# Performance work log

Measured on AMD Instinct MI355X. Metric: run time of the kernel, lower is better.

The kernel has to match this reference:

```python
import jax, jax.numpy as jnp
import numpy as np

GDEP = 3
ALPHA = 0.05
C_IN = 32
C_OUT = 32


def setup_inputs() -> dict:
    key = jax.random.key(0)
    k1, k2, k3, k4 = jax.random.split(key, 4)
    B, C, V, L = 16, C_IN, 512, 168
    x = jax.random.normal(k1, (B, C, V, L), dtype=jnp.float32)
    adj = jax.random.uniform(k2, (V, V), dtype=jnp.float32)
    fan_in = (GDEP + 1) * C_IN  # Conv2d 1x1: kaiming-uniform-ish init
    bound = 1.0 / np.sqrt(fan_in)
    W = jax.random.uniform(k3, (C_OUT, fan_in), minval=-bound, maxval=bound, dtype=jnp.float32)
    b = jax.random.uniform(k4, (C_OUT,), minval=-bound, maxval=bound, dtype=jnp.float32)
    return {"x": x, "adj": adj, "W": W, "b": b}


def reference(x, adj, W, b):
    V = adj.shape[0]
    a = adj + jnp.eye(V, dtype=adj.dtype)
    d = a.sum(axis=1)
    a = a / d[:, None]                      # row-normalized adjacency [V, V]
    h = x
    outs = [h]
    for _ in range(GDEP):                   # small fixed depth loop
        prop = jnp.einsum('ncvl,vw->ncwl', h, a)
        h = ALPHA * x + (1.0 - ALPHA) * prop
        outs.append(h)
    ho = jnp.concatenate(outs, axis=1)      # [B, (gdep+1)*C, V, L]
    # 1x1 conv == channel contraction
    out = jnp.einsum('bcvl,oc->bovl', ho, W) + b[None, :, None, None]
    return out
```

## Files before the change

kernel.cpp:

```cpp
#include <hip/hip_runtime.h>

#define V 512
#define L 168
#define PLANE 86016
#define CHSTRIDE 2752512
#define B_ 16
#define HDR4 (1u << 22)

typedef __attribute__((ext_vector_type(8))) short s16x8;
typedef __attribute__((ext_vector_type(4))) float f32x4;
typedef unsigned short u16;

__device__ inline short f2bf(float f) {
    unsigned u = __builtin_bit_cast(unsigned, f);
    u += 0x7FFF + ((u >> 16) & 1);
    return (short)(u >> 16);
}
__device__ inline float bf2f(u16 s) {
    return __builtin_bit_cast(float, ((unsigned)s) << 16);
}
__device__ inline void gll16(const u16* g, u16* lds) {
    __builtin_amdgcn_global_load_lds(
        (const __attribute__((address_space(1))) void*)g,
        (__attribute__((address_space(3))) void*)lds, 16, 0, 0);
}

__global__ __launch_bounds__(256) void prep2(const float* __restrict__ adj,
                                             const float* __restrict__ W,
                                             u16* __restrict__ M1,
                                             u16* __restrict__ ANb,
                                             u16* __restrict__ Wb) {
    if (blockIdx.x == V) {
        const float al = 0.05f, be = 0.95f;
        for (int i = threadIdx.x; i < 1024; i += 256) {
            const int o = i >> 5, c = i & 31;
            const float w0 = W[o * 128 + c];
            const float w1 = W[o * 128 + 32 + c];
            const float w2 = W[o * 128 + 64 + c];
            const float w3 = W[o * 128 + 96 + c];
            Wb[o * 128 + c]      = f2bf(w0 + al * (w1 + w2 + w3));
            Wb[o * 128 + 32 + c] = f2bf(be * (w1 + al * (w2 + w3)));
            Wb[o * 128 + 64 + c] = f2bf(be * be * (w2 + al * w3));
            Wb[o * 128 + 96 + c] = f2bf(be * be * be * w3);
        }
        return;
    }
    const int v = blockIdx.x;
    float s = 0.f;
    for (int w = threadIdx.x; w < V; w += 256)
        s += adj[v * V + w] + (w == v ? 1.f : 0.f);
    __shared__ float red[256];
    red[threadIdx.x] = s;
    __syncthreads();
    for (int off = 128; off > 0; off >>= 1) {
        if ((int)threadIdx.x < off) red[threadIdx.x] += red[threadIdx.x + off];
        __syncthreads();
    }
    const float inv = 1.f / red[0];
    for (int w = threadIdx.x; w < V; w += 256) {
        const short q = f2bf((adj[v * V + w] + (w == v ? 1.f : 0.f)) * inv);
        M1[w * V + v] = q;
        ANb[v * V + w] = q;
    }
}

__global__ __launch_bounds__(256) void powk(const u16* __restrict__ X,
                                            const u16* __restrict__ ANb,
                                            u16* __restrict__ OUT) {
    const int w0 = (blockIdx.x >> 3) * 64, v0 = (blockIdx.x & 7) * 64;
    const int tid = threadIdx.x, lane = tid & 63, wave = tid >> 6;
    const int colb = lane & 15, kg = lane >> 4;
    f32x4 acc[4];
#pragma unroll
    for (int i = 0; i < 4; i++) acc[i] = (f32x4){0.f, 0.f, 0.f, 0.f};
#pragma unroll 4
    for (int kk = 0; kk < 16; kk++) {
        const int u = kk * 32 + kg * 8;
        const s16x8 bfr = *(const s16x8*)&ANb[(size_t)(v0 + wave * 16 + colb) * 512 + u];
#pragma unroll
        for (int mt = 0; mt < 4; mt++) {
            const s16x8 afr = *(const s16x8*)&X[(size_t)(w0 + mt * 16 + colb) * 512 + u];
            acc[mt] = __builtin_amdgcn_mfma_f32_16x16x32_bf16(afr, bfr, acc[mt], 0, 0, 0);
        }
    }
#pragma unroll
    for (int mt = 0; mt < 4; mt++)
#pragma unroll
        for (int r = 0; r < 4; r++)
            OUT[(size_t)(w0 + mt * 16 + kg * 4 + r) * 512 + v0 + wave * 16 + colb] =
                (u16)f2bf(acc[mt][r]);
}

__global__ __launch_bounds__(256) void cvtT(const float* __restrict__ x,
                                            u16* __restrict__ xa) {
    const int b = blockIdx.z >> 5, c = blockIdx.z & 31;
    const int v0 = blockIdx.y * 64, l0 = blockIdx.x * 64;
    const int tid = threadIdx.x;
    __shared__ float T[64][65];
    const float* xp = x + (size_t)b * CHSTRIDE + (size_t)c * PLANE;
    u16* xo = xa + (size_t)b * CHSTRIDE;
#pragma unroll
    for (int rep = 0; rep < 16; rep++) {
        const int idx = rep * 256 + tid;
        const int vv = idx >> 6, ll = idx & 63;
        if (l0 + ll < L) T[vv][ll] = xp[(size_t)(v0 + vv) * L + l0 + ll];
    }
    __syncthreads();
#pragma unroll
    for (int rep = 0; rep < 16; rep++) {
        const int idx = rep * 256 + tid;
        const int ll = idx >> 6, vv = idx & 63;
        if (l0 + ll < L)
            xo[(size_t)((l0 + ll) * 32 + c) * 512 + v0 + vv] = f2bf(T[vv][ll]);
    }
}

__global__ __launch_bounds__(256, 2) void propOut(const u16* __restrict__ xa,
                                                  const u16* __restrict__ AS,
                                                  const u16* __restrict__ Wb,
                                                  const float* __restrict__ bias,
                                                  u16* __restrict__ tmpb) {
    const int b = blockIdx.z;
    const int logical = (blockIdx.x & 7) * 21 + (blockIdx.x >> 3);
    const int ntile = logical >> 2, wq = logical & 3;
    const int n0 = ntile * 128, w0 = wq * 128, l0 = ntile * 4;
    const int tid = threadIdx.x, lane = tid & 63, wave = tid >> 6;
    const int wm = wave >> 1, wn = wave & 1;
    const int colb = lane & 15, kg = lane >> 4;
    __shared__ __align__(16) u16 SH[2][16384];
    u16* flat = &SH[0][0];
    const size_t sB = (size_t)b * CHSTRIDE;
    const u16* srcb = xa + sB;

    f32x4 aco[2][8];
#pragma unroll
    for (int i = 0; i < 2; i++)
#pragma unroll
        for (int j = 0; j < 8; j++) aco[i][j] = (f32x4){0.f, 0.f, 0.f, 0.f};

#pragma unroll
    for (int pf = 0; pf < 8; pf++) {
        s16x8 bfr;
#pragma unroll
        for (int j = 0; j < 8; j++)
            bfr[j] = (short)srcb[(size_t)(n0 + wave * 32 + kg * 8 + j) * 512 +
                                 w0 + pf * 16 + colb];
#pragma unroll
        for (int mt = 0; mt < 2; mt++) {
            const s16x8 afr = *(const s16x8*)&Wb[(mt * 16 + colb) * 128 + kg * 8];
            aco[mt][pf] = __builtin_amdgcn_mfma_f32_16x16x32_bf16(afr, bfr, aco[mt][pf], 0, 0, 0);
        }
    }

#define STAGE(T, BUF, AK)                                                         \
    {                                                                             \
        const int v0s = (T) * 64;                                                 \
        _Pragma("unroll") for (int i = 0; i < 4; i++) {                           \
            const int cc = wave * 4 + i, oct = cc >> 1, half = cc & 1;            \
            const int row = half * 64 + lane;                                     \
            gll16(&AK[(size_t)(w0 + row) * 512 + v0s + oct * 8],                  \
                  &SH[BUF][oct * 1024 + half * 512]);                             \
            gll16(&srcb[(size_t)(n0 + row) * 512 + v0s + oct * 8],                \
                  &SH[BUF][8192 + oct * 1024 + half * 512]);                      \
        }                                                                         \
    }

#define MFMASTEP(BUF)                                                             \
    _Pragma("unroll") for (int kk = 0; kk < 2; kk++) {                            \
        const int cq = kk * 4 + kg;                                               \
        s16x8 afr[4], bfr[4];                                                     \
        _Pragma("unroll") for (int mt = 0; mt < 4; mt++)                          \
            afr[mt] = *(const s16x8*)&SH[BUF][cq * 1024 +                         \
                                             (wm * 64 + mt * 16 + colb) * 8];     \
        _Pragma("unroll") for (int nt = 0; nt < 4; nt++)                          \
            bfr[nt] = *(const s16x8*)&SH[BUF][8192 + cq * 1024 +                  \
                                             (wn * 64 + nt * 16 + colb) * 8];     \
        _Pragma("unroll") for (int mt = 0; mt < 4; mt++)                          \
            _Pragma("unroll") for (int nt = 0; nt < 4; nt++)                      \
                acc[mt][nt] = __builtin_amdgcn_mfma_f32_16x16x32_bf16(            \
                    afr[mt], bfr[nt], acc[mt][nt], 0, 0, 0);                      \
    }

#define PASS(KP)                                                                  \
    {                                                                             \
        const u16* Ak = AS + (size_t)((KP) - 1) * 262144;                         \
        f32x4 acc[4][4];                                                          \
        _Pragma("unroll") for (int i = 0; i < 4; i++)                             \
            _Pragma("unroll") for (int j = 0; j < 4; j++)                         \
                acc[i][j] = (f32x4){0.f, 0.f, 0.f, 0.f};                          \
        STAGE(0, 0, Ak);                                                          \
        __syncthreads();                                                          \
        _Pragma("unroll") for (int t = 0; t < 8; t++) {                           \
            const int buf = t & 1;                                                \
            if (t < 7) STAGE(t + 1, buf ^ 1, Ak);                                 \
            __builtin_amdgcn_s_setprio(1);                                        \
            MFMASTEP(buf);                                                        \
            __builtin_amdgcn_s_setprio(0);                                        \
            __syncthreads();                                                      \
        }                                                                         \
                              \
        _Pragma("unroll") for (int mt = 0; mt < 4; mt++) {                        \
            const int wr = wm * 64 + mt * 16 + kg * 4;                            \
            _Pragma("unroll") for (int nt = 0; nt < 4; nt++) {                    \
                const int nn = wn * 64 + nt * 16 + colb;                          \
                _Pragma("unroll") for (int r = 0; r < 4; r++)                     \
                    flat[(wr + r) * 136 + nn] = (u16)f2bf(acc[mt][nt][r]);        \
            }                                                                     \
        }                                                                         \
        __syncthreads();                                                          \
                               \
        _Pragma("unroll") for (int pf = 0; pf < 8; pf++) {                        \
            const s16x8 bfr = *(const s16x8*)&flat[(pf * 16 + colb) * 136 +       \
                                                   wave * 32 + kg * 8];           \
            _Pragma("unroll") for (int mt = 0; mt < 2; mt++) {                    \
                const s16x8 afr = *(const s16x8*)&Wb[(mt * 16 + colb) * 128 +     \
                                                     (KP) * 32 + kg * 8];         \
                aco[mt][pf] = __builtin_amdgcn_mfma_f32_16x16x32_bf16(            \
                    afr, bfr, aco[mt][pf], 0, 0, 0);                              \
            }                                                                     \
        }                                                                         \
        __syncthreads();                                                          \
    }

    PASS(1)
    PASS(2)
    PASS(3)
#undef PASS
#undef MFMASTEP
#undef STAGE

#pragma unroll
    for (int mt = 0; mt < 2; mt++)
#pragma unroll
        for (int pf = 0; pf < 8; pf++)
#pragma unroll
            for (int r = 0; r < 4; r++) {
                const int o = mt * 16 + kg * 4 + r;
                tmpb[sB + (size_t)o * PLANE + (size_t)(l0 + wave) * 512 +
                     w0 + pf * 16 + colb] = (u16)f2bf(bias[o] + aco[mt][pf][r]);
            }
}

__global__ __launch_bounds__(256) void transT_b(const u16* __restrict__ tmpb,
                                                float* __restrict__ out) {
    const int o = blockIdx.y, b = blockIdx.z;
    const int vt = blockIdx.x / 3, lt = blockIdx.x % 3;
    const int v0 = vt * 64, l0 = lt * 64;
    const int tid = threadIdx.x;
    __shared__ float T[64][65];
    const u16* tp = tmpb + (size_t)b * CHSTRIDE + (size_t)o * PLANE;
    float* op = out + (size_t)b * CHSTRIDE + (size_t)o * PLANE;
#pragma unroll
    for (int rep = 0; rep < 16; rep++) {
        const int idx = rep * 256 + tid;
        const int ll = idx >> 6, vv = idx & 63;
        if (l0 + ll < L) T[ll][vv] = bf2f(tp[(size_t)(l0 + ll) * 512 + v0 + vv]);
    }
    __syncthreads();
#pragma unroll
    for (int rep = 0; rep < 16; rep++) {
        const int idx = rep * 256 + tid;
        const int vv = idx >> 6, ll = idx & 63;
        if (l0 + ll < L) op[(size_t)(v0 + vv) * L + l0 + ll] = T[ll][vv];
    }
}

extern "C" void kernel_launch(void* const* d_in, const int* in_sizes, int n_in,
                              void* d_out, int out_size, void* d_ws, size_t ws_size,
                              hipStream_t stream) {
    const float* x = (const float*)d_in[0];
    const float* adj = (const float*)d_in[1];
    const float* W = (const float*)d_in[2];
    const float* bias = (const float*)d_in[3];
    float* out = (float*)d_out;

    u16* AS = (u16*)d_ws;
    u16* M1 = AS;
    u16* M2 = AS + 262144;
    u16* M3 = AS + 2 * 262144;
    u16* ANb = AS + 3 * 262144;
    u16* Wb = AS + 4 * 262144;
    u16* hbuf = (u16*)((char*)d_ws + HDR4);

    prep2<<<V + 1, 256, 0, stream>>>(adj, W, M1, ANb, Wb);
    powk<<<64, 256, 0, stream>>>(M1, ANb, M2);
    powk<<<64, 256, 0, stream>>>(M2, ANb, M3);

    const size_t avail = ws_size > HDR4 ? ws_size - HDR4 : 0;
    int nbc = (int)(avail / ((size_t)4 * CHSTRIDE));
    if (nbc < 1) nbc = 1;
    if (nbc > B_) nbc = B_;

    for (int b0 = 0; b0 < B_; b0 += nbc) {
        const int nb = (B_ - b0 < nbc) ? (B_ - b0) : nbc;
        const float* xb = x + (size_t)b0 * CHSTRIDE;
        float* outb = out + (size_t)b0 * CHSTRIDE;
        u16* xa = hbuf;
        u16* tmpb = hbuf + (size_t)nbc * CHSTRIDE;

        cvtT<<<dim3(3, 8, nb * 32), 256, 0, stream>>>(xb, xa);
        propOut<<<dim3(168, 1, nb), 256, 0, stream>>>(xa, AS, Wb, bias, tmpb);
        transT_b<<<dim3(24, 32, nb), 256, 0, stream>>>(tmpb, outb);
    }
}
```

Baseline: 462.2 us.

## Fuse three adjacency-power passes into one K loop sharing the x tile

Replaces the three sequential propagation GEMM passes (one per adjacency power) with a single K loop. Each step loads the x tile once and multiplies it against all three power matrices, accumulating into three register accumulator sets. This cuts global and LDS traffic on the shared operand by a factor of three. In exchange it drops double-buffering, so loads are no longer overlapped with MFMA work, and holding 48 accumulator vectors greatly raises register pressure, which may cause spills or lower occupancy under the 2-blocks-per-CU launch bound.

Measured after the change: 515.8 us. +11.6%, slower.

```diff
diff --git a/kernel.cpp b/kernel.cpp
--- a/kernel.cpp
+++ b/kernel.cpp
@@ -115,11 +115,11 @@
     }
 }
 
-__global__ __launch_bounds__(256, 2) void propOut(const u16* __restrict__ xa,
-                                                  const u16* __restrict__ AS,
-                                                  const u16* __restrict__ Wb,
-                                                  const float* __restrict__ bias,
-                                                  u16* __restrict__ tmpb) {
+__global__ __launch_bounds__(256, 2) void propOut2(const u16* __restrict__ xa,
+                                                   const u16* __restrict__ AS,
+                                                   const u16* __restrict__ Wb,
+                                                   const float* __restrict__ bias,
+                                                   u16* __restrict__ tmpb) {
     const int b = blockIdx.z;
     const int logical = (blockIdx.x & 7) * 21 + (blockIdx.x >> 3);
     const int ntile = logical >> 2, wq = logical & 3;
@@ -127,10 +127,87 @@
     const int tid = threadIdx.x, lane = tid & 63, wave = tid >> 6;
     const int wm = wave >> 1, wn = wave & 1;
     const int colb = lane & 15, kg = lane >> 4;
-    __shared__ __align__(16) u16 SH[2][16384];
-    u16* flat = &SH[0][0];
+    __shared__ __align__(16) u16 SHf[32768];
     const size_t sB = (size_t)b * CHSTRIDE;
     const u16* srcb = xa + sB;
+
+    f32x4 acc1[4][4], acc2[4][4], acc3[4][4];
+#pragma unroll
+    for (int i = 0; i < 4; i++)
+#pragma unroll
+        for (int j = 0; j < 4; j++) {
+            acc1[i][j] = (f32x4){0.f, 0.f, 0.f, 0.f};
+            acc2[i][j] = acc1[i][j];
+            acc3[i][j] = acc1[i][j];
+        }
+
+    const u16* gsrc = (wave == 3) ? srcb + (size_t)n0 * 512
+                                  : AS + (size_t)wave * 262144 + (size_t)w0 * 512;
+    u16* ldst = &SHf[wave * 8192];
+
+    for (int t = 0; t < 8; ++t) {
+        __syncthreads();
+#pragma unroll
+        for (int oh = 0; oh < 16; ++oh) {
+            const int oct = oh >> 1, h = oh & 1;
+            gll16(gsrc + (size_t)(h * 64 + lane) * 512 + t * 64 + oct * 8,
+                  ldst + oct * 1024 + h * 512 + lane * 8);
+        }
+        __syncthreads();
+        __builtin_amdgcn_s_setprio(1);
+#pragma unroll
+        for (int kk = 0; kk < 2; ++kk) {
+            const int cq = kk * 4 + kg;
+            s16x8 bfr[4];
+#pragma unroll
+            for (int nt = 0; nt < 4; nt++)
+                bfr[nt] = *(const s16x8*)&SHf[24576 + cq * 1024 +
+                                              (wn * 64 + nt * 16 + colb) * 8];
+#pragma unroll
+            for (int mt = 0; mt < 4; mt++) {
+                const int aoff = cq * 1024 + (wm * 64 + mt * 16 + colb) * 8;
+                const s16x8 a1 = *(const s16x8*)&SHf[aoff];
+                const s16x8 a2 = *(const s16x8*)&SHf[8192 + aoff];
+                const s16x8 a3 = *(const s16x8*)&SHf[16384 + aoff];
+#pragma unroll
+                for (int nt = 0; nt < 4; nt++) {
+                    acc1[mt][nt] = __builtin_amdgcn_mfma_f32_16x16x32_bf16(a1, bfr[nt],
+                                                                           acc1[mt][nt], 0, 0, 0);
+                    acc2[mt][nt] = __builtin_amdgcn_mfma_f32_16x16x32_bf16(a2, bfr[nt],
+                                                                           acc2[mt][nt], 0, 0, 0);
+                    acc3[mt][nt] = __builtin_amdgcn_mfma_f32_16x16x32_bf16(a3, bfr[nt],
+                                                                           acc3[mt][nt], 0, 0, 0);
+                }
+            }
+        }
+        __builtin_amdgcn_s_setprio(0);
+    }
+
+#define BOUNCE(ACC)                                                               \
+    _Pragma("unroll") for (int mt = 0; mt < 4; mt++) {                            \
+        const int wr = wm * 64 + mt * 16 + kg * 4;                                \
+        _Pragma("unroll") for (int nt = 0; nt < 4; nt++) {                        \
+            const int nn = wn * 64 + nt * 16 + colb;                              \
+            _Pragma("unroll") for (int r = 0; r < 4; r++)                         \
+                SHf[(wr + r) * 136 + nn] = (u16)f2bf(ACC[mt][nt][r]);             \
+        }                                                                         \
+    }
+
+#define OUTACC(KP)                                                                \
+    _Pragma("unroll") for (int pf = 0; pf < 8; pf++) {                            \
+        const s16x8 bfr = *(const s16x8*)&SHf[(pf * 16 + colb) * 136 +            \
+                                              wave * 32 + kg * 8];                \
+        _Pragma("unroll") for (int mt = 0; mt < 2; mt++) {                        \
+            const s16x8 afr = *(const s16x8*)&Wb[(mt * 16 + colb) * 128 +         \
+                                                 (KP) * 32 + kg * 8];             \
+            aco[mt][pf] = __builtin_amdgcn_mfma_f32_16x16x32_bf16(                \
+                afr, bfr, aco[mt][pf], 0, 0, 0);                                  \
+        }                                                                         \
+    }
+
+    __syncthreads();
+    BOUNCE(acc1);
+    __syncthreads();
 
     f32x4 aco[2][8];
 #pragma unroll
@@ -151,83 +228,17 @@
             aco[mt][pf] = __builtin_amdgcn_mfma_f32_16x16x32_bf16(afr, bfr, aco[mt][pf], 0, 0, 0);
         }
     }
-
-#define STAGE(T, BUF, AK)                                                         \
-    {                                                                             \
-        const int v0s = (T) * 64;                                                 \
-        _Pragma("unroll") for (int i = 0; i < 4; i++) {                           \
-            const int cc = wave * 4 + i, oct = cc >> 1, half = cc & 1;            \
-            const int row = half * 64 + lane;                                     \
-            gll16(&AK[(size_t)(w0 + row) * 512 + v0s + oct * 8],                  \
-                  &SH[BUF][oct * 1024 + half * 512]);                             \
-            gll16(&srcb[(size_t)(n0 + row) * 512 + v0s + oct * 8],                \
-                  &SH[BUF][8192 + oct * 1024 + half * 512]);                      \
-        }                                                                         \
-    }
-
-#define MFMASTEP(BUF)                                                             \
-    _Pragma("unroll") for (int kk = 0; kk < 2; kk++) {                            \
-        const int cq = kk * 4 + kg;                                               \
-        s16x8 afr[4], bfr[4];                                                     \
-        _Pragma("unroll") for (int mt = 0; mt < 4; mt++)                          \
-            afr[mt] = *(const s16x8*)&SH[BUF][cq * 1024 +                         \
-                                             (wm * 64 + mt * 16 + colb) * 8];     \
-        _Pragma("unroll") for (int nt = 0; nt < 4; nt++)                          \
-            bfr[nt] = *(const s16x8*)&SH[BUF][8192 + cq * 1024 +                  \
-                                             (wn * 64 + nt * 16 + colb) * 8];     \
-        _Pragma("unroll") for (int mt = 0; mt < 4; mt++)                          \
-            _Pragma("unroll") for (int nt = 0; nt < 4; nt++)                      \
-                acc[mt][nt] = __builtin_amdgcn_mfma_f32_16x16x32_bf16(            \
-                    afr[mt], bfr[nt], acc[mt][nt], 0, 0, 0);                      \
-    }
-
-#define PASS(KP)                                                                  \
-    {                                                                             \
-        const u16* Ak = AS + (size_t)((KP) - 1) * 262144;                         \
-        f32x4 acc[4][4];                                                          \
-        _Pragma("unroll") for (int i = 0; i < 4; i++)                             \
-            _Pragma("unroll") for (int j = 0; j < 4; j++)                         \
-                acc[i][j] = (f32x4){0.f, 0.f, 0.f, 0.f};                          \
-        STAGE(0, 0, Ak);                                                          \
-        __syncthreads();                                                          \
-        _Pragma("unroll") for (int t = 0; t < 8; t++) {                           \
-            const int buf = t & 1;                                                \
-            if (t < 7) STAGE(t + 1, buf ^ 1, Ak);                                 \
-            __builtin_amdgcn_s_setprio(1);                                        \
-            MFMASTEP(buf);                                                        \
-            __builtin_amdgcn_s_setprio(0);                                        \
-            __syncthreads();                                                      \
-        }                                                                         \
-                              \
-        _Pragma("unroll") for (int mt = 0; mt < 4; mt++) {                        \
-            const int wr = wm * 64 + mt * 16 + kg * 4;                            \
-            _Pragma("unroll") for (int nt = 0; nt < 4; nt++) {                    \
-                const int nn = wn * 64 + nt * 16 + colb;                          \
-                _Pragma("unroll") for (int r = 0; r < 4; r++)                     \
-                    flat[(wr + r) * 136 + nn] = (u16)f2bf(acc[mt][nt][r]);        \
-            }                                                                     \
-        }                                                                         \
-        __syncthreads();                                                          \
-                               \
-        _Pragma("unroll") for (int pf = 0; pf < 8; pf++) {                        \
-            const s16x8 bfr = *(const s16x8*)&flat[(pf * 16 + colb) * 136 +       \
-                                                   wave * 32 + kg * 8];           \
-            _Pragma("unroll") for (int mt = 0; mt < 2; mt++) {                    \
-                const s16x8 afr = *(const s16x8*)&Wb[(mt * 16 + colb) * 128 +     \
-                                                     (KP) * 32 + kg * 8];         \
-                aco[mt][pf] = __builtin_amdgcn_mfma_f32_16x16x32_bf16(            \
-                    afr, bfr, aco[mt][pf], 0, 0, 0);                              \
-            }                                                                     \
-        }                                                                         \
-        __syncthreads();                                                          \
-    }
-
-    PASS(1)
-    PASS(2)
-    PASS(3)
-#undef PASS
-#undef MFMASTEP
-#undef STAGE
+    OUTACC(1);
+    __syncthreads();
+    BOUNCE(acc2);
+    __syncthreads();
+    OUTACC(2);
+    __syncthreads();
+    BOUNCE(acc3);
+    __syncthreads();
+    OUTACC(3);
+#undef BOUNCE
+#undef OUTACC
 
 #pragma unroll
     for (int mt = 0; mt < 2; mt++)
@@ -299,7 +310,7 @@
         u16* tmpb = hbuf + (size_t)nbc * CHSTRIDE;
 
         cvtT<<<dim3(3, 8, nb * 32), 256, 0, stream>>>(xb, xa);
-        propOut<<<dim3(168, 1, nb), 256, 0, stream>>>(xa, AS, Wb, bias, tmpb);
+        propOut2<<<dim3(168, 1, nb), 256, 0, stream>>>(xa, AS, Wb, bias, tmpb);
         transT_b<<<dim3(24, 32, nb), 256, 0, stream>>>(tmpb, outb);
     }
 }
```

## Use 32x32x16 MFMA in propagation GEMM and move header into output tail

Applied to the files above, without the earlier changes.

The inner propagation GEMM in propOut now uses 32x32x16 bf16 MFMA tiles instead of 16x16x32, with a 2x2 accumulator layout per wave and a matching scatter into LDS for the fused output projection. The intent is fewer LDS fragment loads per MFMA and better matrix-core throughput. Separately, the small adjacency-power and weight header is moved from the start of the workspace into the tail of the output buffer. That frees the whole workspace for batch chunks, so fewer chunk iterations and launches may be needed. The risk is that the tail of the output, where the header lives, is overwritten by the final transpose. This is only safe because the stream orders the last propOut before that write.

Measured after the change: 464.7 us. About the same (+0.5%).

```diff
diff --git a/kernel.cpp b/kernel.cpp
--- a/kernel.cpp
+++ b/kernel.cpp
@@ -5,10 +5,11 @@
 #define PLANE 86016
 #define CHSTRIDE 2752512
 #define B_ 16
-#define HDR4 (1u << 22)
+#define HDRE 1052672
 
 typedef __attribute__((ext_vector_type(8))) short s16x8;
 typedef __attribute__((ext_vector_type(4))) float f32x4;
+typedef __attribute__((ext_vector_type(16))) float f32x16;
 typedef unsigned short u16;
 
 __device__ inline short f2bf(float f) {
@@ -127,6 +128,7 @@
     const int tid = threadIdx.x, lane = tid & 63, wave = tid >> 6;
     const int wm = wave >> 1, wn = wave & 1;
     const int colb = lane & 15, kg = lane >> 4;
+    const int row31 = lane & 31, kg2 = lane >> 5;
     __shared__ __align__(16) u16 SH[2][16384];
     u16* flat = &SH[0][0];
     const size_t sB = (size_t)b * CHSTRIDE;
@@ -166,28 +168,28 @@
     }
 
 #define MFMASTEP(BUF)                                                             \
-    _Pragma("unroll") for (int kk = 0; kk < 2; kk++) {                            \
-        const int cq = kk * 4 + kg;                                               \
-        s16x8 afr[4], bfr[4];                                                     \
-        _Pragma("unroll") for (int mt = 0; mt < 4; mt++)                          \
-            afr[mt] = *(const s16x8*)&SH[BUF][cq * 1024 +                         \
-                                             (wm * 64 + mt * 16 + colb) * 8];     \
-        _Pragma("unroll") for (int nt = 0; nt < 4; nt++)                          \
-            bfr[nt] = *(const s16x8*)&SH[BUF][8192 + cq * 1024 +                  \
-                                             (wn * 64 + nt * 16 + colb) * 8];     \
-        _Pragma("unroll") for (int mt = 0; mt < 4; mt++)                          \
-            _Pragma("unroll") for (int nt = 0; nt < 4; nt++)                      \
-                acc[mt][nt] = __builtin_amdgcn_mfma_f32_16x16x32_bf16(            \
+    _Pragma("unroll") for (int kk = 0; kk < 4; kk++) {                            \
+        const int koct = kk * 2 + kg2;                                            \
+        s16x8 afr[2], bfr[2];                                                     \
+        _Pragma("unroll") for (int mt = 0; mt < 2; mt++)                          \
+            afr[mt] = *(const s16x8*)&SH[BUF][koct * 1024 +                       \
+                                             (wm * 64 + mt * 32 + row31) * 8];    \
+        _Pragma("unroll") for (int nt = 0; nt < 2; nt++)                          \
+            bfr[nt] = *(const s16x8*)&SH[BUF][8192 + koct * 1024 +                \
+                                             (wn * 64 + nt * 32 + row31) * 8];    \
+        _Pragma("unroll") for (int mt = 0; mt < 2; mt++)                          \
+            _Pragma("unroll") for (int nt = 0; nt < 2; nt++)                      \
+                acc[mt][nt] = __builtin_amdgcn_mfma_f32_32x32x16_bf16(            \
                     afr[mt], bfr[nt], acc[mt][nt], 0, 0, 0);                      \
     }
 
 #define PASS(KP)                                                                  \
     {                                                                             \
         const u16* Ak = AS + (size_t)((KP) - 1) * 262144;                         \
-        f32x4 acc[4][4];                                                          \
-        _Pragma("unroll") for (int i = 0; i < 4; i++)                             \
-            _Pragma("unroll") for (int j = 0; j < 4; j++)                         \
-                acc[i][j] = (f32x4){0.f, 0.f, 0.f, 0.f};                          \
+        f32x16 acc[2][2];                                                         \
+        _Pragma("unroll") for (int i = 0; i < 2; i++)                             \
+            _Pragma("unroll") for (int j = 0; j < 2; j++)                         \
+                acc[i][j] = (f32x16)0.f;                                          \
         STAGE(0, 0, Ak);                                                          \
         __syncthreads();                                                          \
         _Pragma("unroll") for (int t = 0; t < 8; t++) {                           \
@@ -198,17 +200,20 @@
             __builtin_amdgcn_s_setprio(0);                                        \
             __syncthreads();                                                      \
         }                                                                         \
-                              \
-        _Pragma("unroll") for (int mt = 0; mt < 4; mt++) {                        \
-            const int wr = wm * 64 + mt * 16 + kg * 4;                            \
-            _Pragma("unroll") for (int nt = 0; nt < 4; nt++) {                    \
-                const int nn = wn * 64 + nt * 16 + colb;                          \
-                _Pragma("unroll") for (int r = 0; r < 4; r++)                     \
-                    flat[(wr + r) * 136 + nn] = (u16)f2bf(acc[mt][nt][r]);        \
+        \
+        \
+        _Pragma("unroll") for (int mt = 0; mt < 2; mt++) {                        \
+            _Pragma("unroll") for (int nt = 0; nt < 2; nt++) {                    \
+                const int nn = wn * 64 + nt * 32 + row31;                         \
+                _Pragma("unroll") for (int r = 0; r < 16; r++) {                  \
+                    const int wr = wm * 64 + mt * 32 +                            \
+                                   (r & 3) + 8 * (r >> 2) + 4 * kg2;              \
+                    flat[wr * 136 + nn] = (u16)f2bf(acc[mt][nt][r]);              \
+                }                                                                 \
             }                                                                     \
         }                                                                         \
         __syncthreads();                                                          \
-                               \
+           \
         _Pragma("unroll") for (int pf = 0; pf < 8; pf++) {                        \
             const s16x8 bfr = *(const s16x8*)&flat[(pf * 16 + colb) * 136 +       \
                                                    wave * 32 + kg * 8];           \
@@ -274,20 +279,20 @@
     const float* bias = (const float*)d_in[3];
     float* out = (float*)d_out;
 
-    u16* AS = (u16*)d_ws;
+    u16* hdr = (u16*)((char*)d_out + (size_t)out_size * 4 - (size_t)HDRE * 2 - 256);
+    u16* AS = hdr;
     u16* M1 = AS;
     u16* M2 = AS + 262144;
     u16* M3 = AS + 2 * 262144;
     u16* ANb = AS + 3 * 262144;
     u16* Wb = AS + 4 * 262144;
-    u16* hbuf = (u16*)((char*)d_ws + HDR4);
+    u16* hbuf = (u16*)d_ws;
 
     prep2<<<V + 1, 256, 0, stream>>>(adj, W, M1, ANb, Wb);
     powk<<<64, 256, 0, stream>>>(M1, ANb, M2);
     powk<<<64, 256, 0, stream>>>(M2, ANb, M3);
 
-    const size_t avail = ws_size > HDR4 ? ws_size - HDR4 : 0;
-    int nbc = (int)(avail / ((size_t)4 * CHSTRIDE));
+    int nbc = (int)(ws_size / ((size_t)4 * CHSTRIDE));
     if (nbc < 1) nbc = 1;
     if (nbc > B_) nbc = B_;
 
```
